# Performance work log

Hardware: AMD Instinct MI355X
Metric: run time of the kernel (lower is better)

Reference implementation:

```python
import jax, jax.numpy as jnp
import numpy as np

B, C, H, W = 8, 3, 1024, 1024


def _cubic_weights(t):
    # Catmull-Rom-style weights used by the torch module
    t2 = t * t
    t3 = t2 * t
    cm1 = (-t3 + 2.0 * t2 - t) / 2.0
    c0 = (3.0 * t3 - 5.0 * t2 + 2.0) / 2.0
    c1 = (-3.0 * t3 + 4.0 * t2 + t) / 2.0
    c2 = 1.0 - (cm1 + c0 + c1)
    return (cm1, c0, c1, c2)


def setup_inputs() -> dict:
    key = jax.random.key(0)
    k1, k2, k3 = jax.random.split(key, 3)
    input_image = jax.random.uniform(k1, (B, C, H, W), dtype=jnp.float32)
    delta_x = jax.random.normal(k2, (B, C, H, W), dtype=jnp.float32)
    delta_y = jax.random.normal(k3, (B, C, H, W), dtype=jnp.float32)
    return {"input_image": input_image, "delta_x": delta_x, "delta_y": delta_y}


def reference(input_image, delta_x, delta_y):
    Bb, Cc, Hh, Ww = input_image.shape
    BXC = Bb * Cc
    # base integer grid, broadcast over (B, C)
    Xg = jnp.arange(Ww, dtype=jnp.float32)          # [W]
    Yg = jnp.arange(Hh, dtype=jnp.float32)[:, None]  # [H,1]
    # normalized coords as in the torch module, then back to pixel coords
    new_X = (Xg + delta_x - Ww / 2.0) / (Ww / 2.0 - 1.0)
    new_Y = (Yg + delta_y - Hh / 2.0) / (Hh / 2.0 - 1.0)
    x_map = (new_X + 1.0) * (Ww - 1) / 2.0  # [B,C,H,W]
    y_map = (new_Y + 1.0) * (Hh - 1) / 2.0

    x0f = jnp.floor(x_map)
    y0f = jnp.floor(y_map)
    tx = x_map - x0f
    ty = y_map - y0f
    x0 = x0f.astype(jnp.int32)
    y0 = y0f.astype(jnp.int32)

    wx = [w.reshape(BXC, Hh * Ww) for w in _cubic_weights(tx)]
    wy = [w.reshape(BXC, Hh * Ww) for w in _cubic_weights(ty)]
    xs = [jnp.clip(x0 + o, 0, Ww - 1).reshape(BXC, Hh * Ww) for o in (-1, 0, 1, 2)]
    ys = [jnp.clip(y0 + o, 0, Hh - 1).reshape(BXC, Hh * Ww) for o in (-1, 0, 1, 2)]

    img = input_image.reshape(BXC, Hh * Ww)
    out = jnp.zeros((BXC, Hh * Ww), dtype=jnp.float32)
    for j in range(4):  # fixed 4x4 taps
        row = jnp.zeros((BXC, Hh * Ww), dtype=jnp.float32)
        yoff = ys[j] * Ww
        for i in range(4):
            vals = jnp.take_along_axis(img, yoff + xs[i], axis=1)
            row = row + wx[i] * vals
        out = out + wy[j] * row
    out = jnp.clip(out, 0.0, 1.0)
    return out.reshape(Bb, Cc, Hh, Ww)
```

## Files before the change

kernel.cpp:

```cpp
#include <hip/hip_runtime.h>


#define HD 1024
#define WD 1024
#define TILE 64
#define HALOX 8
#define HALOY 6
#define SROWS 76
#define DSTR 64
#define COFF 4864

typedef __attribute__((ext_vector_type(2))) _Float16 f16x2;
typedef __attribute__((ext_vector_type(2))) __fp16   h16x2;
typedef __attribute__((ext_vector_type(2))) float    f32x2;

__device__ __forceinline__ float cubic_gather_global(
    const float* __restrict__ p, int x0, int y0,
    float wxm1, float wx0, float wx1, float wx2,
    float wym1, float wy0, float wy1, float wy2)
{
    int cx0 = min(max(x0 - 1, 0), WD - 1);
    int cx1 = min(max(x0,     0), WD - 1);
    int cx2 = min(max(x0 + 1, 0), WD - 1);
    int cx3 = min(max(x0 + 2, 0), WD - 1);
    int cy0 = min(max(y0 - 1, 0), HD - 1);
    int cy1 = min(max(y0,     0), HD - 1);
    int cy2 = min(max(y0 + 1, 0), HD - 1);
    int cy3 = min(max(y0 + 2, 0), HD - 1);
    const float* r0 = p + (size_t)cy0 * WD;
    const float* r1 = p + (size_t)cy1 * WD;
    const float* r2 = p + (size_t)cy2 * WD;
    const float* r3 = p + (size_t)cy3 * WD;
    float s0 = wxm1 * r0[cx0] + wx0 * r0[cx1] + wx1 * r0[cx2] + wx2 * r0[cx3];
    float s1 = wxm1 * r1[cx0] + wx0 * r1[cx1] + wx1 * r1[cx2] + wx2 * r1[cx3];
    float s2 = wxm1 * r2[cx0] + wx0 * r2[cx1] + wx1 * r2[cx2] + wx2 * r2[cx3];
    float s3 = wxm1 * r3[cx0] + wx0 * r3[cx1] + wx1 * r3[cx2] + wx2 * r3[cx3];
    return wym1 * s0 + wy0 * s1 + wy1 * s2 + wy2 * s3;
}

__device__ __forceinline__ uint32_t pk16(float a, float b) {
    h16x2 h = __builtin_amdgcn_cvt_pkrtz(a, b);
    return __builtin_bit_cast(uint32_t, h);
}
__device__ __forceinline__ f16x2 u2h(uint32_t u) {
    return __builtin_bit_cast(f16x2, u);
}

__global__ __launch_bounds__(256) void bicubic_tile_kernel(
    const float* __restrict__ img,
    const float* __restrict__ dxp,
    const float* __restrict__ dyp,
    float* __restrict__ out)
{
    __shared__ uint32_t smp[2 * COFF];

    const int bx = blockIdx.x * TILE;
    const int by = blockIdx.y * TILE;
    const int plane = blockIdx.z;
    const float* __restrict__ p = img + (size_t)plane * (size_t)(HD * WD);

    const int gx0 = bx - HALOX;
    const int gy0 = by - HALOY;
    const int tid = threadIdx.x;

    if (gx0 >= 0 && gx0 + 80 <= WD - 1) {
        for (int s = tid; s < SROWS * 20; s += 256) {
            int r = s / 20;
            int q = s - r * 20;
            int gy = min(max(gy0 + r, 0), HD - 1);
            const float* rowp = p + (size_t)gy * WD + gx0;
            float4 v = *reinterpret_cast<const float4*>(rowp + 4 * q);
            float v4 = rowp[4 * q + 4];
            int b = r * DSTR + 2 * q;
            smp[b]            = pk16(v.x, v.y);
            smp[b + 1]        = pk16(v.z, v.w);
            smp[COFF + b]     = pk16(v.y, v.z);
            smp[COFF + b + 1] = pk16(v.w, v4);
        }
    } else {
        for (int s = tid; s < SROWS * 40; s += 256) {
            int r = s / 40;
            int j = s - r * 40;
            int gy = min(max(gy0 + r, 0), HD - 1);
            const float* rowp = p + (size_t)gy * WD;
            int e0 = min(max(gx0 + 2 * j,     0), WD - 1);
            int e1 = min(max(gx0 + 2 * j + 1, 0), WD - 1);
            int e2 = min(max(gx0 + 2 * j + 2, 0), WD - 1);
            float v0 = rowp[e0], v1 = rowp[e1], v2 = rowp[e2];
            int b = r * DSTR + j;
            smp[b]        = pk16(v0, v1);
            smp[COFF + b] = pk16(v1, v2);
        }
    }
    __syncthreads();

    const int col = bx + (tid & 63);
    const int rbase = by + (tid >> 6);
    const int didx0 = (plane << 20) | (rbase << 10) | col;

    float vdx[16], vdy[16];
    #pragma unroll
    for (int it = 0; it < 16; ++it) {
        vdx[it] = dxp[didx0 + it * 4096];
        vdy[it] = dyp[didx0 + it * 4096];
    }

    const float sc = 511.5f / 511.0f;
    const float colA = ((float)col - 512.0f) * sc + 511.5f;
    const float yA0 = ((float)rbase - 512.0f) * sc + 511.5f;
    const float yStep = 4.0f * sc;

    const f32x2 cN05 = {-0.5f, -0.5f};
    const f32x2 cP05 = { 0.5f,  0.5f};
    const f32x2 cP1  = { 1.0f,  1.0f};
    const f32x2 cN1  = {-1.0f, -1.0f};
    const f32x2 cP2  = { 2.0f,  2.0f};
    const f32x2 cN25 = {-2.5f, -2.5f};
    const f32x2 cP15 = { 1.5f,  1.5f};
    const f32x2 cN15 = {-1.5f, -1.5f};

    #pragma unroll
    for (int it = 0; it < 16; ++it) {
        const int didx = didx0 + it * 4096;
        const float ddx = vdx[it];
        const float ddy = vdy[it];

        float x_map = fmaf(ddx, sc, colA);
        float y_map = fmaf(ddy, sc, yA0 + (float)it * yStep);

        float x0f = floorf(x_map);
        float y0f = floorf(y_map);
        int x0 = (int)x0f;
        int y0 = (int)y0f;

        f32x2 t;
        t.x = x_map - x0f;
        t.y = y_map - y0f;
        f32x2 t2v = t * t;
        f32x2 t3v = t2v * t;
        f32x2 wm1 = __builtin_elementwise_fma(t3v, cN05,
                        __builtin_elementwise_fma(t, cN05, t2v));
        f32x2 w0v = __builtin_elementwise_fma(t3v, cP15,
                        __builtin_elementwise_fma(t2v, cN25, cP1));
        f32x2 w1v = __builtin_elementwise_fma(t3v, cN15,
                        __builtin_elementwise_fma(t2v, cP2, t * cP05));
        f32x2 w2v = __builtin_elementwise_fma(wm1 + w0v + w1v, cN1, cP1);

        const int lx = x0 - 1 - gx0;
        const int ly = y0 - 1 - gy0;
        const bool inb = ((unsigned)lx <= 76u) & ((unsigned)ly <= 72u);

        float acc;
        if (inb) {
            f16x2 wxa = u2h(pk16(wm1.x, w0v.x));
            f16x2 wxb = u2h(pk16(w1v.x, w2v.x));
            const int base = ((lx & 1) ? COFF : 0) + ly * DSTR + (lx >> 1);
            uint32_t a0 = smp[base],            a1 = smp[base + 1];
            uint32_t b0 = smp[base + DSTR],     b1 = smp[base + DSTR + 1];
            uint32_t c0 = smp[base + 2 * DSTR], c1 = smp[base + 2 * DSTR + 1];
            uint32_t d0 = smp[base + 3 * DSTR], d1 = smp[base + 3 * DSTR + 1];
            float s0 = __builtin_amdgcn_fdot2(wxa, u2h(a0),
                         __builtin_amdgcn_fdot2(wxb, u2h(a1), 0.0f, false), false);
            float s1 = __builtin_amdgcn_fdot2(wxa, u2h(b0),
                         __builtin_amdgcn_fdot2(wxb, u2h(b1), 0.0f, false), false);
            float s2 = __builtin_amdgcn_fdot2(wxa, u2h(c0),
                         __builtin_amdgcn_fdot2(wxb, u2h(c1), 0.0f, false), false);
            float s3 = __builtin_amdgcn_fdot2(wxa, u2h(d0),
                         __builtin_amdgcn_fdot2(wxb, u2h(d1), 0.0f, false), false);
            acc = wm1.y * s0 + w0v.y * s1 + w1v.y * s2 + w2v.y * s3;
        } else {
            acc = cubic_gather_global(p, x0, y0, wm1.x, w0v.x, w1v.x, w2v.x,
                                      wm1.y, w0v.y, w1v.y, w2v.y);
        }
        out[didx] = fminf(fmaxf(acc, 0.0f), 1.0f);
    }
}

extern "C" void kernel_launch(void* const* d_in, const int* in_sizes, int n_in,
                              void* d_out, int out_size, void* d_ws, size_t ws_size,
                              hipStream_t stream) {
    const float* img = (const float*)d_in[0];
    const float* dxp = (const float*)d_in[1];
    const float* dyp = (const float*)d_in[2];
    float* out = (float*)d_out;

    const int planes = in_sizes[0] / (HD * WD);
    dim3 grid(WD / TILE, HD / TILE, planes);
    bicubic_tile_kernel<<<grid, 256, 0, stream>>>(img, dxp, dyp, out);
}
```

Measured before the change: 100.1 us.

## Pack vertical pixel pairs in shared memory instead of duplicated horizontal pairs

Replaces the two shifted copies of horizontally packed fp16 pairs with a single array where each word packs a pixel with the one below it, at row stride 96. The interpolation now does the vertical weighting with fdot2 and the horizontal weighting in fp32. This roughly halves the shared-memory footprint and the duplicate packing stores, and removes the odd/even column branch. The cost is loading each global row twice during staging and a different LDS bank-access pattern for the eight reads per pixel.

```diff
diff --git a/kernel.cpp b/kernel.cpp
--- a/kernel.cpp
+++ b/kernel.cpp
@@ -6,9 +6,9 @@
 #define TILE 64
 #define HALOX 8
 #define HALOY 6
-#define SROWS 76
-#define DSTR 64
-#define COFF 4864
+#define PROWS 75
+#define SCOLS 80
+#define DSTR 96
 
 typedef __attribute__((ext_vector_type(2))) _Float16 f16x2;
 typedef __attribute__((ext_vector_type(2))) __fp16   h16x2;
@@ -52,7 +52,7 @@
     const float* __restrict__ dyp,
     float* __restrict__ out)
 {
-    __shared__ uint32_t smp[2 * COFF];
+    __shared__ uint32_t smp[PROWS * DSTR];
 
     const int bx = blockIdx.x * TILE;
     const int by = blockIdx.y * TILE;
@@ -63,33 +63,31 @@
     const int gy0 = by - HALOY;
     const int tid = threadIdx.x;
 
-    if (gx0 >= 0 && gx0 + 80 <= WD - 1) {
-        for (int s = tid; s < SROWS * 20; s += 256) {
+    if (gx0 >= 0 && gx0 + SCOLS <= WD) {
+        for (int s = tid; s < PROWS * 20; s += 256) {
             int r = s / 20;
             int q = s - r * 20;
-            int gy = min(max(gy0 + r, 0), HD - 1);
-            const float* rowp = p + (size_t)gy * WD + gx0;
-            float4 v = *reinterpret_cast<const float4*>(rowp + 4 * q);
-            float v4 = rowp[4 * q + 4];
-            int b = r * DSTR + 2 * q;
-            smp[b]            = pk16(v.x, v.y);
-            smp[b + 1]        = pk16(v.z, v.w);
-            smp[COFF + b]     = pk16(v.y, v.z);
-            smp[COFF + b + 1] = pk16(v.w, v4);
+            int gya = min(max(gy0 + r,     0), HD - 1);
+            int gyb = min(max(gy0 + r + 1, 0), HD - 1);
+            const float* ra = p + (size_t)gya * WD + gx0;
+            const float* rb = p + (size_t)gyb * WD + gx0;
+            float4 a = *reinterpret_cast<const float4*>(ra + 4 * q);
+            float4 b = *reinterpret_cast<const float4*>(rb + 4 * q);
+            int o = r * DSTR + 4 * q;
+            smp[o + 0] = pk16(a.x, b.x);
+            smp[o + 1] = pk16(a.y, b.y);
+            smp[o + 2] = pk16(a.z, b.z);
+            smp[o + 3] = pk16(a.w, b.w);
         }
     } else {
-        for (int s = tid; s < SROWS * 40; s += 256) {
-            int r = s / 40;
-            int j = s - r * 40;
-            int gy = min(max(gy0 + r, 0), HD - 1);
-            const float* rowp = p + (size_t)gy * WD;
-            int e0 = min(max(gx0 + 2 * j,     0), WD - 1);
-            int e1 = min(max(gx0 + 2 * j + 1, 0), WD - 1);
-            int e2 = min(max(gx0 + 2 * j + 2, 0), WD - 1);
-            float v0 = rowp[e0], v1 = rowp[e1], v2 = rowp[e2];
-            int b = r * DSTR + j;
-            smp[b]        = pk16(v0, v1);
-            smp[COFF + b] = pk16(v1, v2);
+        for (int s = tid; s < PROWS * SCOLS; s += 256) {
+            int r = s / SCOLS;
+            int c = s - r * SCOLS;
+            int gya = min(max(gy0 + r,     0), HD - 1);
+            int gyb = min(max(gy0 + r + 1, 0), HD - 1);
+            int e = min(max(gx0 + c, 0), WD - 1);
+            smp[r * DSTR + c] = pk16(p[(size_t)gya * WD + e],
+                                     p[(size_t)gyb * WD + e]);
         }
     }
     __syncthreads();
@@ -148,26 +146,27 @@
 
         const int lx = x0 - 1 - gx0;
         const int ly = y0 - 1 - gy0;
-        const bool inb = ((unsigned)lx <= 76u) & ((unsigned)ly <= 72u);
+        const bool inb = ((unsigned)lx <= (unsigned)(SCOLS - 4)) &
+                         ((unsigned)ly <= (unsigned)(PROWS - 3));
 
         float acc;
         if (inb) {
-            f16x2 wxa = u2h(pk16(wm1.x, w0v.x));
-            f16x2 wxb = u2h(pk16(w1v.x, w2v.x));
-            const int base = ((lx & 1) ? COFF : 0) + ly * DSTR + (lx >> 1);
-            uint32_t a0 = smp[base],            a1 = smp[base + 1];
-            uint32_t b0 = smp[base + DSTR],     b1 = smp[base + DSTR + 1];
-            uint32_t c0 = smp[base + 2 * DSTR], c1 = smp[base + 2 * DSTR + 1];
-            uint32_t d0 = smp[base + 3 * DSTR], d1 = smp[base + 3 * DSTR + 1];
-            float s0 = __builtin_amdgcn_fdot2(wxa, u2h(a0),
-                         __builtin_amdgcn_fdot2(wxb, u2h(a1), 0.0f, false), false);
-            float s1 = __builtin_amdgcn_fdot2(wxa, u2h(b0),
-                         __builtin_amdgcn_fdot2(wxb, u2h(b1), 0.0f, false), false);
-            float s2 = __builtin_amdgcn_fdot2(wxa, u2h(c0),
-                         __builtin_amdgcn_fdot2(wxb, u2h(c1), 0.0f, false), false);
-            float s3 = __builtin_amdgcn_fdot2(wxa, u2h(d0),
-                         __builtin_amdgcn_fdot2(wxb, u2h(d1), 0.0f, false), false);
-            acc = wm1.y * s0 + w0v.y * s1 + w1v.y * s2 + w2v.y * s3;
+            f16x2 wya = u2h(pk16(wm1.y, w0v.y));
+            f16x2 wyb = u2h(pk16(w1v.y, w2v.y));
+            const int base = ly * DSTR + lx;
+            uint32_t u0 = smp[base + 0], v0 = smp[base + 2 * DSTR + 0];
+            uint32_t u1 = smp[base + 1], v1 = smp[base + 2 * DSTR + 1];
+            uint32_t u2 = smp[base + 2], v2 = smp[base + 2 * DSTR + 2];
+            uint32_t u3 = smp[base + 3], v3 = smp[base + 2 * DSTR + 3];
+            float c0 = __builtin_amdgcn_fdot2(wya, u2h(u0),
+                         __builtin_amdgcn_fdot2(wyb, u2h(v0), 0.0f, false), false);
+            float c1 = __builtin_amdgcn_fdot2(wya, u2h(u1),
+                         __builtin_amdgcn_fdot2(wyb, u2h(v1), 0.0f, false), false);
+            float c2 = __builtin_amdgcn_fdot2(wya, u2h(u2),
+                         __builtin_amdgcn_fdot2(wyb, u2h(v2), 0.0f, false), false);
+            float c3 = __builtin_amdgcn_fdot2(wya, u2h(u3),
+                         __builtin_amdgcn_fdot2(wyb, u2h(v3), 0.0f, false), false);
+            acc = wm1.x * c0 + w0v.x * c1 + w1v.x * c2 + w2v.x * c3;
         } else {
             acc = cubic_gather_global(p, x0, y0, wm1.x, w0v.x, w1v.x, w2v.x,
                                       wm1.y, w0v.y, w1v.y, w2v.y);
```

New measurement: 112.1 us. 12.0% more time.
